# Kernel optimization log

Hardware: AMD Instinct MI355X
Metric: run time of the kernel (lower is better)

Reference implementation:

```python
import jax, jax.numpy as jnp
import numpy as np

B, NA, NT, P, DA, DM, H = 1, 4096, 1024, 32768, 128, 512, 4
DH = DA // H
DF = 4 * DA
WINDOW = 16


def _layer_norm(x, g=None, b=None, eps=1e-5):
    m = jnp.mean(x, axis=-1, keepdims=True)
    v = jnp.var(x, axis=-1, keepdims=True)
    xn = (x - m) / jnp.sqrt(v + eps)
    if g is not None:
        xn = xn * g + b
    return xn


def setup_inputs() -> dict:
    key = jax.random.key(0)
    ks = jax.random.split(key, 32)
    r = lambda k, s: (jax.random.normal(k, s, dtype=jnp.float32) * 0.05)
    return {
        'q': r(ks[0], (B, NA, DA)),
        'c_atom': r(ks[1], (B, NA, DA)),
        'h_cond': r(ks[2], (B, NT, DM)),
        'p_lm': r(ks[3], (B, P, 16)),
        't_emb': r(ks[4], (B, DA)),
        'cond_proj_w': r(ks[5], (DM, DA)), 'cond_proj_b': r(ks[6], (DA,)),
        'adaln1_w': r(ks[7], (DA, 2 * DA)), 'adaln1_b': r(ks[8], (2 * DA,)),
        'adaln2_w': r(ks[9], (DA, 2 * DA)), 'adaln2_b': r(ks[10], (2 * DA,)),
        'ln_g': jnp.ones((DA,), jnp.float32), 'ln_b': jnp.zeros((DA,), jnp.float32),
        'wq': r(ks[11], (DA, DA)), 'wk': r(ks[12], (DA, DA)),
        'wv': r(ks[13], (DA, DA)), 'wg': r(ks[14], (DA, DA)),
        'wo': r(ks[15], (DA, DA)),
        'pair_w': r(ks[16], (16, H)), 'pair_b': r(ks[17], (H,)),
        'gate1_w': r(ks[18], (DA, DA)), 'gate1_b': r(ks[19], (DA,)),
        'gate2_w': r(ks[20], (DA, DA)), 'gate2_b': r(ks[21], (DA,)),
        'sw1': r(ks[22], (DA, DF)), 'sw3': r(ks[23], (DA, DF)),
        'sw2': r(ks[24], (DF, DA)),
        'p_lm_idx': jax.random.randint(ks[25], (B, P, 2), 0, NA, dtype=jnp.int32),
        'token_idx': jnp.sort(jax.random.randint(ks[26], (B, NA), 0, NT, dtype=jnp.int32), axis=-1),
    }


def _forward(q, c_atom, h_cond, p_lm, t_emb,
             cond_proj_w, cond_proj_b, adaln1_w, adaln1_b, adaln2_w, adaln2_b,
             ln_g, ln_b, wq, wk, wv, wg, wo, pair_w, pair_b,
             gate1_w, gate1_b, gate2_w, gate2_b, sw1, sw3, sw2,
             p_lm_idx, token_idx):
    Bq, N, D = q.shape
    # gather token conditioning to atoms: (B, NA, DM)
    h_atoms = jax.vmap(lambda h, t: h[t])(h_cond, token_idx)
    cond = t_emb[:, None, :] + h_atoms @ cond_proj_w + cond_proj_b  # (B, NA, DA)
    g1, b1 = jnp.split(cond @ adaln1_w + adaln1_b, 2, axis=-1)
    q_n = (1.0 + g1) * _layer_norm(q, ln_g, ln_b) + b1

    Q = (q_n @ wq).reshape(Bq, N, H, DH)
    K = (q_n @ wk).reshape(Bq, N, H, DH)
    V = (q_n @ wv).reshape(Bq, N, H, DH)
    G_flat = q_n @ wg  # (B, N, DA); permute/reshape in torch is identity on layout

    scores = jnp.einsum('bihd,bjhd->bhij', Q, K) / jnp.sqrt(jnp.float32(DH))

    # scattered pair bias: (B, P, H) -> dense (B, H, N, N)
    bias = p_lm @ pair_w + pair_b  # (B, P, H)

    def scat(idx, bb):
        return jnp.zeros((N, N, H), bb.dtype).at[idx[:, 0], idx[:, 1]].set(bb)

    pair_bias = jax.vmap(scat)(p_lm_idx, bias).transpose(0, 3, 1, 2)
    scores = scores + pair_bias

    pos = jnp.arange(N)
    window = jnp.abs(pos[:, None] - pos[None, :]) <= WINDOW  # (N, N)
    scores = jnp.where(window[None, None, :, :], scores, -jnp.inf)

    attn = jax.nn.softmax(scores, axis=-1)
    att_out = jnp.einsum('bhij,bjhd->bihd', attn, V).reshape(Bq, N, D)

    q1 = q + jax.nn.sigmoid(G_flat) * (att_out @ wo)
    q1 = q1 + jax.nn.sigmoid(c_atom @ gate1_w + gate1_b) * q1

    g2, b2 = jnp.split(cond @ adaln2_w + adaln2_b, 2, axis=-1)
    q_n2 = (1.0 + g2) * _layer_norm(q1) + b2
    swi = (jax.nn.silu(q_n2 @ sw1) * (q_n2 @ sw3)) @ sw2
    q2 = q1 + jax.nn.sigmoid(c_atom @ gate2_w + gate2_b) * swi
    return q2  # atom_pad_mask is all-ones -> final mask multiply is identity


def reference(q, c_atom, h_cond, p_lm, t_emb,
              cond_proj_w, cond_proj_b, adaln1_w, adaln1_b, adaln2_w, adaln2_b,
              ln_g, ln_b, wq, wk, wv, wg, wo, pair_w, pair_b,
              gate1_w, gate1_b, gate2_w, gate2_b, sw1, sw3, sw2,
              p_lm_idx, token_idx):
    return _forward(q, c_atom, h_cond, p_lm, t_emb,
                    cond_proj_w, cond_proj_b, adaln1_w, adaln1_b, adaln2_w, adaln2_b,
                    ln_g, ln_b, wq, wk, wv, wg, wo, pair_w, pair_b,
                    gate1_w, gate1_b, gate2_w, gate2_b, sw1, sw3, sw2,
                    p_lm_idx, token_idx)
```

## Files before the change

### kernel.cpp

```cpp
#include <hip/hip_runtime.h>
#include <math.h>

#define NA   4096
#define DA   128
#define DM   512
#define NT   1024
#define HH   4
#define DF   512
#define PP   32768
#define WIN  16
#define BAND 33

typedef __attribute__((ext_vector_type(8))) short bf16x8;
typedef __attribute__((ext_vector_type(4))) float f32x4;

__device__ __forceinline__ float sigmoidf_(float x) { return 1.0f / (1.0f + __expf(-x)); }
__device__ __forceinline__ ushort f2bf(float f) {
    union { float f; unsigned int i; } x; x.f = f;
    unsigned int r = x.i + 0x7fffu + ((x.i >> 16) & 1u);
    return (ushort)(r >> 16);
}

template<int K, int NF>
__device__ __forceinline__ void gemm_core(
    const ushort* __restrict__ Arow, const ushort* __restrict__ WTcol,
    f32x4* acc, int ko)
{
    #pragma unroll
    for (int ks = 0; ks < K / 32; ++ks) {
        bf16x8 a = *(const bf16x8*)(Arow + ks * 32 + ko);
        #pragma unroll
        for (int nf = 0; nf < NF; ++nf) {
            bf16x8 b = *(const bf16x8*)(WTcol + (size_t)nf * 16 * K + ks * 32 + ko);
            acc[nf] = __builtin_amdgcn_mfma_f32_16x16x32_bf16(a, b, acc[nf], 0, 0, 0);
        }
    }
}

__global__ __launch_bounds__(256) void k_prep(
    const float* __restrict__ hc, const float* __restrict__ ca,
    const float* __restrict__ cw, const float* __restrict__ a1, const float* __restrict__ a2,
    const float* __restrict__ wq, const float* __restrict__ wk, const float* __restrict__ wv,
    const float* __restrict__ wg, const float* __restrict__ wo,
    const float* __restrict__ g1, const float* __restrict__ g2,
    const float* __restrict__ s1, const float* __restrict__ s3, const float* __restrict__ s2,
    ushort* hcb, ushort* cab, ushort* cwT, ushort* a1T, ushort* a2T,
    ushort* wqT, ushort* wkT, ushort* wvT, ushort* wgT, ushort* woT,
    ushort* g1T, ushort* g2T, ushort* s1T, ushort* s3T, ushort* s2T,
    float* band, float* outz)
{
    __shared__ float tile[32][33];
    const int y = blockIdx.y, bx = blockIdx.x, tid = threadIdx.x;
    if (y <= 1) {
        const float4* src = (const float4*)(y == 0 ? hc : ca);
        ushort* dst = y == 0 ? hcb : cab;
        for (int i = bx * 256 + tid; i < 131072; i += 16384) {
            float4 v = src[i];
            ushort4 st; st.x = f2bf(v.x); st.y = f2bf(v.y); st.z = f2bf(v.z); st.w = f2bf(v.w);
            *(ushort4*)&dst[(size_t)i * 4] = st;
        }
        return;
    }
    if (y == 15) {
        float4 z = {0.f, 0.f, 0.f, 0.f};
        float4* b4 = (float4*)band;
        for (int i = bx * 256 + tid; i < 135168; i += 16384) b4[i] = z;
        return;
    }
    if (y == 16) {
        float4 z = {0.f, 0.f, 0.f, 0.f};
        float4* o4 = (float4*)outz;
        for (int i = bx * 256 + tid; i < 131072; i += 16384) o4[i] = z;
        return;
    }
    const float* src; ushort* dst; int K, N;
    switch (y) {
        case 2:  src = cw; dst = cwT; K = 512; N = 128; break;
        case 3:  src = a1; dst = a1T; K = 128; N = 256; break;
        case 4:  src = a2; dst = a2T; K = 128; N = 256; break;
        case 5:  src = wq; dst = wqT; K = 128; N = 128; break;
        case 6:  src = wk; dst = wkT; K = 128; N = 128; break;
        case 7:  src = wv; dst = wvT; K = 128; N = 128; break;
        case 8:  src = wg; dst = wgT; K = 128; N = 128; break;
        case 9:  src = wo; dst = woT; K = 128; N = 128; break;
        case 10: src = g1; dst = g1T; K = 128; N = 128; break;
        case 11: src = g2; dst = g2T; K = 128; N = 128; break;
        case 12: src = s1; dst = s1T; K = 128; N = 512; break;
        case 13: src = s3; dst = s3T; K = 128; N = 512; break;
        default: src = s2; dst = s2T; K = 512; N = 128; break;
    }
    const int tn_cnt = N >> 5;
    if (bx >= (K >> 5) * tn_cnt) return;
    const int k0 = (bx / tn_cnt) << 5, n0 = (bx % tn_cnt) << 5;
    {
        int r = tid >> 3, c = (tid & 7) << 2;
        float4 v = *(const float4*)&src[(size_t)(k0 + r) * N + n0 + c];
        tile[r][c + 0] = v.x; tile[r][c + 1] = v.y;
        tile[r][c + 2] = v.z; tile[r][c + 3] = v.w;
    }
    __syncthreads();
    {
        int rn = tid >> 3, ck = (tid & 7) << 2;
        ushort4 st;
        st.x = f2bf(tile[ck + 0][rn]);
        st.y = f2bf(tile[ck + 1][rn]);
        st.z = f2bf(tile[ck + 2][rn]);
        st.w = f2bf(tile[ck + 3][rn]);
        *(ushort4*)&dst[(size_t)(n0 + rn) * K + k0 + ck] = st;
    }
}

__global__ __launch_bounds__(256) void k_cond(
    const ushort* __restrict__ hcb, const int* __restrict__ tok,
    const ushort* __restrict__ cwT, const float* __restrict__ t_emb,
    const float* __restrict__ cond_b, ushort* __restrict__ cond_bf,
    const float* __restrict__ p_lm, const float* __restrict__ pair_w,
    const float* __restrict__ pair_b, const int* __restrict__ p_idx,
    float* __restrict__ band)
{
    const int tid = threadIdx.x, y = blockIdx.y;
    if (y >= 4) {
        int p = ((y - 4) * 64 + blockIdx.x) * 256 + tid;
        int i = p_idx[2 * p], j = p_idx[2 * p + 1];
        int d = j - i + WIN;
        if (d < 0 || d > 2 * WIN) return;
        float v0 = pair_b[0], v1 = pair_b[1], v2 = pair_b[2], v3 = pair_b[3];
        #pragma unroll
        for (int k = 0; k < 16; ++k) {
            float a = p_lm[p * 16 + k];
            v0 = fmaf(a, pair_w[k * 4 + 0], v0);
            v1 = fmaf(a, pair_w[k * 4 + 1], v1);
            v2 = fmaf(a, pair_w[k * 4 + 2], v2);
            v3 = fmaf(a, pair_w[k * 4 + 3], v3);
        }
        size_t base = ((size_t)i * HH) * BAND + d;
        band[base + 0 * BAND] = v0;
        band[base + 1 * BAND] = v1;
        band[base + 2 * BAND] = v2;
        band[base + 3 * BAND] = v3;
        return;
    }
    const int l = tid & 63, w = tid >> 6, cl = l & 15, ko = (l >> 4) * 8;
    const int m0 = blockIdx.x * 64, n0 = y * 32;
    const int trow = tok[m0 + w * 16 + cl];
    f32x4 acc[2] = {};
    gemm_core<512, 2>(hcb + (size_t)trow * DM, cwT + (size_t)(n0 + cl) * DM, acc, ko);
    const int r0 = m0 + w * 16 + (l >> 4) * 4;
    #pragma unroll
    for (int nf = 0; nf < 2; ++nf) {
        int col = n0 + nf * 16 + cl;
        float add = t_emb[col] + cond_b[col];
        #pragma unroll
        for (int r = 0; r < 4; ++r)
            cond_bf[(size_t)(r0 + r) * DA + col] = f2bf(acc[nf][r] + add);
    }
}

__global__ __launch_bounds__(256) void k_modgate(
    const ushort* __restrict__ cond_bf, const ushort* __restrict__ cab,
    const ushort* __restrict__ a1T, const ushort* __restrict__ a2T,
    const ushort* __restrict__ g1T, const ushort* __restrict__ g2T,
    const float* __restrict__ ad1b, const float* __restrict__ ad2b,
    const float* __restrict__ g1b, const float* __restrict__ g2b,
    float* __restrict__ gb1, float* __restrict__ gb2,
    float* __restrict__ gate1, float* __restrict__ gate2)
{
    const int tid = threadIdx.x, y = blockIdx.y;
    const int l = tid & 63, w = tid >> 6, cl = l & 15, ko = (l >> 4) * 8;
    const int m0 = blockIdx.x * 64;
    const ushort* A; const ushort* WT; const float* bias; float* O; int ldo, n0, sig;
    if (y < 4)       { A = cond_bf; WT = a1T; bias = ad1b; O = gb1;   ldo = 256; n0 = y * 64;        sig = 0; }
    else if (y < 8)  { A = cond_bf; WT = a2T; bias = ad2b; O = gb2;   ldo = 256; n0 = (y - 4) * 64;  sig = 0; }
    else if (y < 10) { A = cab;     WT = g1T; bias = g1b;  O = gate1; ldo = 128; n0 = (y - 8) * 64;  sig = 1; }
    else             { A = cab;     WT = g2T; bias = g2b;  O = gate2; ldo = 128; n0 = (y - 10) * 64; sig = 1; }
    f32x4 acc[4] = {};
    gemm_core<128, 4>(A + (size_t)(m0 + w * 16 + cl) * DA, WT + (size_t)(n0 + cl) * DA, acc, ko);
    const int r0 = m0 + w * 16 + (l >> 4) * 4;
    #pragma unroll
    for (int nf = 0; nf < 4; ++nf) {
        int col = n0 + nf * 16 + cl;
        float bb = bias[col];
        #pragma unroll
        for (int r = 0; r < 4; ++r) {
            float v = acc[nf][r] + bb;
            if (sig) v = sigmoidf_(v);
            O[(size_t)(r0 + r) * ldo + col] = v;
        }
    }
}

__global__ __launch_bounds__(256) void k_qkvg(
    const float* __restrict__ q, const float* __restrict__ gb1,
    const float* __restrict__ ln_g, const float* __restrict__ ln_b,
    const ushort* __restrict__ wqT, const ushort* __restrict__ wkT,
    const ushort* __restrict__ wvT, const ushort* __restrict__ wgT,
    float* __restrict__ Qb, float* __restrict__ Kb,
    float* __restrict__ Vb, float* __restrict__ sG)
{
    const int tid = threadIdx.x, l = tid & 63, w = tid >> 6;
    const int cl = l & 15, kq = l >> 4, ko = kq * 8;
    const int m0 = blockIdx.x * 64, n0 = blockIdx.y * 64, z = blockIdx.z;
    const int row = m0 + w * 16 + cl;

    float qv[4][8];
    float sum = 0.f, sq = 0.f;
    #pragma unroll
    for (int ks = 0; ks < 4; ++ks) {
        float4 v0 = *(const float4*)&q[(size_t)row * DA + ks * 32 + ko];
        float4 v1 = *(const float4*)&q[(size_t)row * DA + ks * 32 + ko + 4];
        qv[ks][0] = v0.x; qv[ks][1] = v0.y; qv[ks][2] = v0.z; qv[ks][3] = v0.w;
        qv[ks][4] = v1.x; qv[ks][5] = v1.y; qv[ks][6] = v1.z; qv[ks][7] = v1.w;
        sum += v0.x + v0.y + v0.z + v0.w + v1.x + v1.y + v1.z + v1.w;
        sq += v0.x * v0.x + v0.y * v0.y + v0.z * v0.z + v0.w * v0.w
            + v1.x * v1.x + v1.y * v1.y + v1.z * v1.z + v1.w * v1.w;
    }
    sum += __shfl_xor(sum, 16); sq += __shfl_xor(sq, 16);
    sum += __shfl_xor(sum, 32); sq += __shfl_xor(sq, 32);
    float mean = sum * (1.0f / DA);
    float rs = rsqrtf(sq * (1.0f / DA) - mean * mean + 1e-5f);

    bf16x8 afr[4];
    #pragma unroll
    for (int ks = 0; ks < 4; ++ks) {
        int k = ks * 32 + ko;
        float4 lg0 = *(const float4*)&ln_g[k], lg1 = *(const float4*)&ln_g[k + 4];
        float4 lb0 = *(const float4*)&ln_b[k], lb1 = *(const float4*)&ln_b[k + 4];
        float4 g0 = *(const float4*)&gb1[(size_t)row * 256 + k];
        float4 g1v = *(const float4*)&gb1[(size_t)row * 256 + k + 4];
        float4 b0 = *(const float4*)&gb1[(size_t)row * 256 + 128 + k];
        float4 b1v = *(const float4*)&gb1[(size_t)row * 256 + 128 + k + 4];
        float lg[8] = {lg0.x, lg0.y, lg0.z, lg0.w, lg1.x, lg1.y, lg1.z, lg1.w};
        float lb[8] = {lb0.x, lb0.y, lb0.z, lb0.w, lb1.x, lb1.y, lb1.z, lb1.w};
        float gg[8] = {g0.x, g0.y, g0.z, g0.w, g1v.x, g1v.y, g1v.z, g1v.w};
        float bb[8] = {b0.x, b0.y, b0.z, b0.w, b1v.x, b1v.y, b1v.z, b1v.w};
        #pragma unroll
        for (int j = 0; j < 8; ++j) {
            float xn = (qv[ks][j] - mean) * rs;
            float yv = (1.f + gg[j]) * (xn * lg[j] + lb[j]) + bb[j];
            afr[ks][j] = (short)f2bf(yv);
        }
    }

    const ushort* WT = (z == 0) ? wqT : (z == 1) ? wkT : (z == 2) ? wvT : wgT;
    float* O = (z == 0) ? Qb : (z == 1) ? Kb : (z == 2) ? Vb : sG;
    const ushort* Wc = WT + (size_t)(n0 + cl) * DA;
    f32x4 acc[4] = {};
    #pragma unroll
    for (int ks = 0; ks < 4; ++ks) {
        #pragma unroll
        for (int nf = 0; nf < 4; ++nf) {
            bf16x8 b = *(const bf16x8*)(Wc + (size_t)nf * 16 * DA + ks * 32 + ko);
            acc[nf] = __builtin_amdgcn_mfma_f32_16x16x32_bf16(afr[ks], b, acc[nf], 0, 0, 0);
        }
    }
    const int r0 = m0 + w * 16 + kq * 4;
    #pragma unroll
    for (int nf = 0; nf < 4; ++nf) {
        int col = n0 + nf * 16 + cl;
        #pragma unroll
        for (int r = 0; r < 4; ++r) {
            float v = acc[nf][r];
            if (z == 3) v = sigmoidf_(v);
            O[(size_t)(r0 + r) * DA + col] = v;
        }
    }
}

__global__ __launch_bounds__(512) void k_attnwo(
    const float* __restrict__ Qb, const float* __restrict__ Kb,
    const float* __restrict__ Vb, const float* __restrict__ band,
    const float* __restrict__ q, const float* __restrict__ sG,
    const float* __restrict__ gate1, const ushort* __restrict__ woT,
    float* __restrict__ q1)
{
    __shared__ ushort att_s[16 * 128];
    const int tid = threadIdx.x;
    const int r0 = blockIdx.x * 16;
    {
        const int g = tid >> 3, l3 = tid & 7;
        const int rl = g >> 2, h = g & 3;
        const int i = r0 + rl;
        const float scale = 0.17677669529663687f;
        float4 qr = *(const float4*)(Qb + (size_t)i * DA + h * 32 + l3 * 4);
        const float* brow = band + ((size_t)i * HH + h) * BAND;
        float s[BAND];
        float m = -1e30f;
        #pragma unroll
        for (int jo = 0; jo < BAND; ++jo) {
            int j = i - WIN + jo;
            float sv = -1e30f;
            if ((unsigned)j < NA) {
                float4 kk = *(const float4*)(Kb + (size_t)j * DA + h * 32 + l3 * 4);
                float d = 0.f;
                d = fmaf(qr.x, kk.x, d); d = fmaf(qr.y, kk.y, d);
                d = fmaf(qr.z, kk.z, d); d = fmaf(qr.w, kk.w, d);
                d += __shfl_xor(d, 1);
                d += __shfl_xor(d, 2);
                d += __shfl_xor(d, 4);
                sv = fmaf(d, scale, brow[jo]);
            }
            s[jo] = sv;
            m = fmaxf(m, sv);
        }
        float lsum = 0.f;
        #pragma unroll
        for (int jo = 0; jo < BAND; ++jo) {
            float p = __expf(s[jo] - m);
            s[jo] = p;
            lsum += p;
        }
        float inv = 1.0f / lsum;
        float4 o = {0.f, 0.f, 0.f, 0.f};
        #pragma unroll
        for (int jo = 0; jo < BAND; ++jo) {
            int j = i - WIN + jo;
            if ((unsigned)j < NA) {
                float4 v = *(const float4*)(Vb + (size_t)j * DA + h * 32 + l3 * 4);
                o.x = fmaf(s[jo], v.x, o.x);
                o.y = fmaf(s[jo], v.y, o.y);
                o.z = fmaf(s[jo], v.z, o.z);
                o.w = fmaf(s[jo], v.w, o.w);
            }
        }
        ushort4 st;
        st.x = f2bf(o.x * inv); st.y = f2bf(o.y * inv);
        st.z = f2bf(o.z * inv); st.w = f2bf(o.w * inv);
        int byte = rl * 256 + h * 64 + l3 * 8;
        byte ^= (rl & 7) << 4;
        *(ushort4*)((char*)att_s + byte) = st;
    }
    __syncthreads();
    {
        const int l = tid & 63, w = tid >> 6;
        const int cl = l & 15, kq = l >> 4, ko = kq * 8;
        const int n0 = w * 16;
        f32x4 acc = {0.f, 0.f, 0.f, 0.f};
        #pragma unroll
        for (int ks = 0; ks < 4; ++ks) {
            int byteA = cl * 256 + (ks * 32 + ko) * 2;
            byteA ^= (cl & 7) << 4;
            bf16x8 a = *(const bf16x8*)((char*)att_s + byteA);
            bf16x8 b = *(const bf16x8*)(woT + (size_t)(n0 + cl) * DA + ks * 32 + ko);
            acc = __builtin_amdgcn_mfma_f32_16x16x32_bf16(a, b, acc, 0, 0, 0);
        }
        #pragma unroll
        for (int r = 0; r < 4; ++r) {
            int row = r0 + kq * 4 + r, col = n0 + cl;
            size_t rc = (size_t)row * DA + col;
            q1[rc] = (q[rc] + sG[rc] * acc[r]) * (1.f + gate1[rc]);
        }
    }
}

__global__ __launch_bounds__(256) void k_ffn(
    const float* __restrict__ q1, const float* __restrict__ gb2,
    const float* __restrict__ gate2,
    const ushort* __restrict__ s1T, const ushort* __restrict__ s3T,
    const ushort* __restrict__ s2T, float* __restrict__ out)
{
    __shared__ ushort hbs[16 * 128];
    const int tid = threadIdx.x, l = tid & 63, w = tid >> 6;
    const int cl = l & 15, kq = l >> 4, ko = kq * 8;
    const int m0 = blockIdx.x * 16;
    const int by = blockIdx.y;
    const int row = m0 + cl;

    float qv[4][8];
    float sum = 0.f, sq = 0.f;
    #pragma unroll
    for (int ks = 0; ks < 4; ++ks) {
        float4 v0 = *(const float4*)&q1[(size_t)row * DA + ks * 32 + ko];
        float4 v1 = *(const float4*)&q1[(size_t)row * DA + ks * 32 + ko + 4];
        qv[ks][0] = v0.x; qv[ks][1] = v0.y; qv[ks][2] = v0.z; qv[ks][3] = v0.w;
        qv[ks][4] = v1.x; qv[ks][5] = v1.y; qv[ks][6] = v1.z; qv[ks][7] = v1.w;
        sum += v0.x + v0.y + v0.z + v0.w + v1.x + v1.y + v1.z + v1.w;
        sq += v0.x * v0.x + v0.y * v0.y + v0.z * v0.z + v0.w * v0.w
            + v1.x * v1.x + v1.y * v1.y + v1.z * v1.z + v1.w * v1.w;
    }
    sum += __shfl_xor(sum, 16); sq += __shfl_xor(sq, 16);
    sum += __shfl_xor(sum, 32); sq += __shfl_xor(sq, 32);
    float mean = sum * (1.0f / DA);
    float rs = rsqrtf(sq * (1.0f / DA) - mean * mean + 1e-5f);

    bf16x8 afr[4];
    #pragma unroll
    for (int ks = 0; ks < 4; ++ks) {
        int k = ks * 32 + ko;
        float4 g0 = *(const float4*)&gb2[(size_t)row * 256 + k];
        float4 g1v = *(const float4*)&gb2[(size_t)row * 256 + k + 4];
        float4 b0 = *(const float4*)&gb2[(size_t)row * 256 + 128 + k];
        float4 b1v = *(const float4*)&gb2[(size_t)row * 256 + 128 + k + 4];
        float gg[8] = {g0.x, g0.y, g0.z, g0.w, g1v.x, g1v.y, g1v.z, g1v.w};
        float bb[8] = {b0.x, b0.y, b0.z, b0.w, b1v.x, b1v.y, b1v.z, b1v.w};
        #pragma unroll
        for (int j = 0; j < 8; ++j) {
            float xn = (qv[ks][j] - mean) * rs;
            afr[ks][j] = (short)f2bf((1.f + gg[j]) * xn + bb[j]);
        }
    }

    {
        const ushort* W1 = s1T + (size_t)(by * 128 + w * 32 + cl) * DA;
        const ushort* W3 = s3T + (size_t)(by * 128 + w * 32 + cl) * DA;
        f32x4 acc1[2] = {}, acc3[2] = {};
        #pragma unroll
        for (int ks = 0; ks < 4; ++ks) {
            #pragma unroll
            for (int nf = 0; nf < 2; ++nf) {
                bf16x8 b1 = *(const bf16x8*)(W1 + (size_t)nf * 16 * DA + ks * 32 + ko);
                acc1[nf] = __builtin_amdgcn_mfma_f32_16x16x32_bf16(afr[ks], b1, acc1[nf], 0, 0, 0);
                bf16x8 b3 = *(const bf16x8*)(W3 + (size_t)nf * 16 * DA + ks * 32 + ko);
                acc3[nf] = __builtin_amdgcn_mfma_f32_16x16x32_bf16(afr[ks], b3, acc3[nf], 0, 0, 0);
            }
        }
        #pragma unroll
        for (int nf = 0; nf < 2; ++nf) {
            #pragma unroll
            for (int r = 0; r < 4; ++r) {
                float x1 = acc1[nf][r], x3 = acc3[nf][r];
                float h = x1 * sigmoidf_(x1) * x3;
                int rr = kq * 4 + r;
                int col = w * 32 + nf * 16 + cl;
                int byte = rr * 256 + col * 2;
                byte ^= (rr & 7) << 4;
                *(ushort*)((char*)hbs + byte) = f2bf(h);
            }
        }
    }
    __syncthreads();
    {
        const ushort* W2 = s2T + (size_t)(w * 32 + cl) * DF + by * 128;
        f32x4 acc[2] = {};
        #pragma unroll
        for (int ks = 0; ks < 4; ++ks) {
            int byteA = cl * 256 + (ks * 32 + ko) * 2;
            byteA ^= (cl & 7) << 4;
            bf16x8 a = *(const bf16x8*)((char*)hbs + byteA);
            #pragma unroll
            for (int nf = 0; nf < 2; ++nf) {
                bf16x8 b = *(const bf16x8*)(W2 + (size_t)nf * 16 * DF + ks * 32 + ko);
                acc[nf] = __builtin_amdgcn_mfma_f32_16x16x32_bf16(a, b, acc[nf], 0, 0, 0);
            }
        }
        #pragma unroll
        for (int nf = 0; nf < 2; ++nf) {
            #pragma unroll
            for (int r = 0; r < 4; ++r) {
                int rowg = m0 + kq * 4 + r, col = w * 32 + nf * 16 + cl;
                size_t rc = (size_t)rowg * DA + col;
                float val = gate2[rc] * acc[nf][r];
                if (by == 0) val += q1[rc];
                atomicAdd(&out[rc], val);
            }
        }
    }
}

extern "C" void kernel_launch(void* const* d_in, const int* in_sizes, int n_in,
                              void* d_out, int out_size, void* d_ws, size_t ws_size,
                              hipStream_t stream)
{
    const float* q      = (const float*)d_in[0];
    const float* c_atom = (const float*)d_in[1];
    const float* h_cond = (const float*)d_in[2];
    const float* p_lm   = (const float*)d_in[3];
    const float* t_emb  = (const float*)d_in[4];
    const float* cond_w = (const float*)d_in[5];
    const float* cond_b = (const float*)d_in[6];
    const float* ad1w   = (const float*)d_in[7];
    const float* ad1b   = (const float*)d_in[8];
    const float* ad2w   = (const float*)d_in[9];
    const float* ad2b   = (const float*)d_in[10];
    const float* ln_g   = (const float*)d_in[11];
    const float* ln_b   = (const float*)d_in[12];
    const float* wq     = (const float*)d_in[13];
    const float* wk     = (const float*)d_in[14];
    const float* wv     = (const float*)d_in[15];
    const float* wg     = (const float*)d_in[16];
    const float* wo     = (const float*)d_in[17];
    const float* pair_w = (const float*)d_in[18];
    const float* pair_b = (const float*)d_in[19];
    const float* g1w    = (const float*)d_in[20];
    const float* g1b    = (const float*)d_in[21];
    const float* g2w    = (const float*)d_in[22];
    const float* g2b    = (const float*)d_in[23];
    const float* sw1    = (const float*)d_in[24];
    const float* sw3    = (const float*)d_in[25];
    const float* sw2    = (const float*)d_in[26];
    const int*   p_idx  = (const int*)d_in[27];
    const int*   tok    = (const int*)d_in[28];
    float* out = (float*)d_out;

    size_t off = 0;
    char* base = (char*)d_ws;
    auto alloc = [&](size_t bytes) -> void* {
        void* p = base + off;
        off += (bytes + 255) & ~(size_t)255;
        return p;
    };
    ushort* hcb     = (ushort*)alloc((size_t)NT * DM * 2);
    ushort* cab     = (ushort*)alloc((size_t)NA * DA * 2);
    ushort* cwT     = (ushort*)alloc((size_t)DM * DA * 2);
    ushort* a1T     = (ushort*)alloc((size_t)256 * 128 * 2);
    ushort* a2T     = (ushort*)alloc((size_t)256 * 128 * 2);
    ushort* wqT     = (ushort*)alloc((size_t)128 * 128 * 2);
    ushort* wkT     = (ushort*)alloc((size_t)128 * 128 * 2);
    ushort* wvT     = (ushort*)alloc((size_t)128 * 128 * 2);
    ushort* wgT     = (ushort*)alloc((size_t)128 * 128 * 2);
    ushort* woT     = (ushort*)alloc((size_t)128 * 128 * 2);
    ushort* g1T     = (ushort*)alloc((size_t)128 * 128 * 2);
    ushort* g2T     = (ushort*)alloc((size_t)128 * 128 * 2);
    ushort* s1T     = (ushort*)alloc((size_t)512 * 128 * 2);
    ushort* s3T     = (ushort*)alloc((size_t)512 * 128 * 2);
    ushort* s2T     = (ushort*)alloc((size_t)128 * 512 * 2);
    ushort* cond_bf = (ushort*)alloc((size_t)NA * DA * 2);
    float*  gb1     = (float*)alloc((size_t)NA * 256 * 4);
    float*  gb2     = (float*)alloc((size_t)NA * 256 * 4);
    float*  gate1   = (float*)alloc((size_t)NA * DA * 4);
    float*  gate2   = (float*)alloc((size_t)NA * DA * 4);
    float*  Qb      = (float*)alloc((size_t)NA * DA * 4);
    float*  Kb      = (float*)alloc((size_t)NA * DA * 4);
    float*  Vb      = (float*)alloc((size_t)NA * DA * 4);
    float*  sG      = (float*)alloc((size_t)NA * DA * 4);
    float*  band    = (float*)alloc((size_t)NA * HH * BAND * 4);
    float*  q1      = (float*)alloc((size_t)NA * DA * 4);

    k_prep<<<dim3(64, 17), 256, 0, stream>>>(
        h_cond, c_atom, cond_w, ad1w, ad2w, wq, wk, wv, wg, wo,
        g1w, g2w, sw1, sw3, sw2,
        hcb, cab, cwT, a1T, a2T, wqT, wkT, wvT, wgT, woT,
        g1T, g2T, s1T, s3T, s2T, band, out);
    k_cond<<<dim3(64, 6), 256, 0, stream>>>(hcb, tok, cwT, t_emb, cond_b, cond_bf,
                                            p_lm, pair_w, pair_b, p_idx, band);
    k_modgate<<<dim3(64, 12), 256, 0, stream>>>(cond_bf, cab, a1T, a2T, g1T, g2T,
                                                ad1b, ad2b, g1b, g2b,
                                                gb1, gb2, gate1, gate2);
    k_qkvg<<<dim3(64, 2, 4), 256, 0, stream>>>(q, gb1, ln_g, ln_b,
                                               wqT, wkT, wvT, wgT, Qb, Kb, Vb, sG);
    k_attnwo<<<NA / 16, 512, 0, stream>>>(Qb, Kb, Vb, band, q, sG, gate1, woT, q1);
    k_ffn<<<dim3(NA / 16, 4), 256, 0, stream>>>(q1, gb2, gate2, s1T, s3T, s2T, out);
    (void)in_sizes; (void)n_in; (void)out_size; (void)ws_size;
}
```

Before: 198.8 us.

## Store intermediates in bf16, split LN kernel, fuse modgate pairs, drop FFN atomics

Converts the modulation, gate and sigmoid-gate buffers from fp32 to bf16, which halves their memory traffic. The layer norm moves out of k_qkvg into a separate k_ln1 kernel that writes a bf16 normalized tensor, so the four projection blocks stop recomputing it. k_modgate now computes paired GEMMs that share one A row. k_ffn becomes a single 512-thread block per 16 rows that does all of DF, removing the output zeroing pass and the atomicAdd reduction, in exchange for less grid parallelism, an extra launch and bf16 rounding error.

```diff
diff --git a/kernel.cpp b/kernel.cpp
--- a/kernel.cpp
+++ b/kernel.cpp
@@ -20,21 +20,9 @@
     unsigned int r = x.i + 0x7fffu + ((x.i >> 16) & 1u);
     return (ushort)(r >> 16);
 }
-
-template<int K, int NF>
-__device__ __forceinline__ void gemm_core(
-    const ushort* __restrict__ Arow, const ushort* __restrict__ WTcol,
-    f32x4* acc, int ko)
-{
-    #pragma unroll
-    for (int ks = 0; ks < K / 32; ++ks) {
-        bf16x8 a = *(const bf16x8*)(Arow + ks * 32 + ko);
-        #pragma unroll
-        for (int nf = 0; nf < NF; ++nf) {
-            bf16x8 b = *(const bf16x8*)(WTcol + (size_t)nf * 16 * K + ks * 32 + ko);
-            acc[nf] = __builtin_amdgcn_mfma_f32_16x16x32_bf16(a, b, acc[nf], 0, 0, 0);
-        }
-    }
+__device__ __forceinline__ float bf2f(ushort u) {
+    union { unsigned int i; float f; } x; x.i = ((unsigned int)u) << 16;
+    return x.f;
 }
 
 __global__ __launch_bounds__(256) void k_prep(
@@ -47,7 +35,7 @@
     ushort* hcb, ushort* cab, ushort* cwT, ushort* a1T, ushort* a2T,
     ushort* wqT, ushort* wkT, ushort* wvT, ushort* wgT, ushort* woT,
     ushort* g1T, ushort* g2T, ushort* s1T, ushort* s3T, ushort* s2T,
-    float* band, float* outz)
+    float* band)
 {
     __shared__ float tile[32][33];
     const int y = blockIdx.y, bx = blockIdx.x, tid = threadIdx.x;
@@ -65,12 +53,6 @@
         float4 z = {0.f, 0.f, 0.f, 0.f};
         float4* b4 = (float4*)band;
         for (int i = bx * 256 + tid; i < 135168; i += 16384) b4[i] = z;
-        return;
-    }
-    if (y == 16) {
-        float4 z = {0.f, 0.f, 0.f, 0.f};
-        float4* o4 = (float4*)outz;
-        for (int i = bx * 256 + tid; i < 131072; i += 16384) o4[i] = z;
         return;
     }
     const float* src; ushort* dst; int K, N;
@@ -110,6 +92,22 @@
     }
 }
 
+template<int K, int NF>
+__device__ __forceinline__ void gemm_core(
+    const ushort* __restrict__ Arow, const ushort* __restrict__ WTcol,
+    f32x4* acc, int ko)
+{
+    #pragma unroll
+    for (int ks = 0; ks < K / 32; ++ks) {
+        bf16x8 a = *(const bf16x8*)(Arow + ks * 32 + ko);
+        #pragma unroll
+        for (int nf = 0; nf < NF; ++nf) {
+            bf16x8 b = *(const bf16x8*)(WTcol + (size_t)nf * 16 * K + ks * 32 + ko);
+            acc[nf] = __builtin_amdgcn_mfma_f32_16x16x32_bf16(a, b, acc[nf], 0, 0, 0);
+        }
+    }
+}
+
 __global__ __launch_bounds__(256) void k_cond(
     const ushort* __restrict__ hcb, const int* __restrict__ tok,
     const ushort* __restrict__ cwT, const float* __restrict__ t_emb,
@@ -162,106 +160,106 @@
     const ushort* __restrict__ g1T, const ushort* __restrict__ g2T,
     const float* __restrict__ ad1b, const float* __restrict__ ad2b,
     const float* __restrict__ g1b, const float* __restrict__ g2b,
-    float* __restrict__ gb1, float* __restrict__ gb2,
-    float* __restrict__ gate1, float* __restrict__ gate2)
+    ushort* __restrict__ gb1, ushort* __restrict__ gb2,
+    ushort* __restrict__ gate1, ushort* __restrict__ gate2)
 {
     const int tid = threadIdx.x, y = blockIdx.y;
     const int l = tid & 63, w = tid >> 6, cl = l & 15, ko = (l >> 4) * 8;
     const int m0 = blockIdx.x * 64;
-    const ushort* A; const ushort* WT; const float* bias; float* O; int ldo, n0, sig;
-    if (y < 4)       { A = cond_bf; WT = a1T; bias = ad1b; O = gb1;   ldo = 256; n0 = y * 64;        sig = 0; }
-    else if (y < 8)  { A = cond_bf; WT = a2T; bias = ad2b; O = gb2;   ldo = 256; n0 = (y - 4) * 64;  sig = 0; }
-    else if (y < 10) { A = cab;     WT = g1T; bias = g1b;  O = gate1; ldo = 128; n0 = (y - 8) * 64;  sig = 1; }
-    else             { A = cab;     WT = g2T; bias = g2b;  O = gate2; ldo = 128; n0 = (y - 10) * 64; sig = 1; }
-    f32x4 acc[4] = {};
-    gemm_core<128, 4>(A + (size_t)(m0 + w * 16 + cl) * DA, WT + (size_t)(n0 + cl) * DA, acc, ko);
+    const int gatep = (y >= 4);
+    const int n0 = gatep ? (y - 4) * 64 : y * 64;
+    const ushort* A  = gatep ? cab : cond_bf;
+    const ushort* W1 = gatep ? g1T : a1T;
+    const ushort* W2 = gatep ? g2T : a2T;
+    const float* b1 = gatep ? g1b : ad1b;
+    const float* b2 = gatep ? g2b : ad2b;
+    ushort* O1 = gatep ? gate1 : gb1;
+    ushort* O2 = gatep ? gate2 : gb2;
+    const int ldo = gatep ? DA : 256;
+
+    const ushort* Arow = A + (size_t)(m0 + w * 16 + cl) * DA;
+    const ushort* W1c = W1 + (size_t)(n0 + cl) * DA;
+    const ushort* W2c = W2 + (size_t)(n0 + cl) * DA;
+    f32x4 acc1[4] = {}, acc2[4] = {};
+    #pragma unroll
+    for (int ks = 0; ks < 4; ++ks) {
+        bf16x8 a = *(const bf16x8*)(Arow + ks * 32 + ko);
+        #pragma unroll
+        for (int nf = 0; nf < 4; ++nf) {
+            bf16x8 w1v = *(const bf16x8*)(W1c + (size_t)nf * 16 * DA + ks * 32 + ko);
+            acc1[nf] = __builtin_amdgcn_mfma_f32_16x16x32_bf16(a, w1v, acc1[nf], 0, 0, 0);
+            bf16x8 w2v = *(const bf16x8*)(W2c + (size_t)nf * 16 * DA + ks * 32 + ko);
+            acc2[nf] = __builtin_amdgcn_mfma_f32_16x16x32_bf16(a, w2v, acc2[nf], 0, 0, 0);
+        }
+    }
     const int r0 = m0 + w * 16 + (l >> 4) * 4;
     #pragma unroll
     for (int nf = 0; nf < 4; ++nf) {
         int col = n0 + nf * 16 + cl;
-        float bb = bias[col];
+        float bb1 = b1[col], bb2 = b2[col];
         #pragma unroll
         for (int r = 0; r < 4; ++r) {
-            float v = acc[nf][r] + bb;
-            if (sig) v = sigmoidf_(v);
-            O[(size_t)(r0 + r) * ldo + col] = v;
-        }
-    }
+            float v1 = acc1[nf][r] + bb1;
+            float v2 = acc2[nf][r] + bb2;
+            if (gatep) { v1 = sigmoidf_(v1); v2 = sigmoidf_(v2); }
+            O1[(size_t)(r0 + r) * ldo + col] = f2bf(v1);
+            O2[(size_t)(r0 + r) * ldo + col] = f2bf(v2);
+        }
+    }
+}
+
+__global__ __launch_bounds__(256) void k_ln1(
+    const float* __restrict__ q, const ushort* __restrict__ gb1,
+    const float* __restrict__ ln_g, const float* __restrict__ ln_b,
+    ushort* __restrict__ qn_bf)
+{
+    const int w = threadIdx.x >> 6, l = threadIdx.x & 63;
+    const int row = blockIdx.x * 4 + w;
+    float2 xv = *(const float2*)&q[(size_t)row * DA + 2 * l];
+    float sum = xv.x + xv.y, sq = xv.x * xv.x + xv.y * xv.y;
+    #pragma unroll
+    for (int off = 1; off <= 32; off <<= 1) {
+        sum += __shfl_xor(sum, off);
+        sq  += __shfl_xor(sq,  off);
+    }
+    float m = sum * (1.0f / DA);
+    float rs = rsqrtf(sq * (1.0f / DA) - m * m + 1e-5f);
+    ushort2 gu = *(const ushort2*)&gb1[(size_t)row * 256 + 2 * l];
+    ushort2 bu = *(const ushort2*)&gb1[(size_t)row * 256 + 128 + 2 * l];
+    float2 lg = *(const float2*)&ln_g[2 * l];
+    float2 lb = *(const float2*)&ln_b[2 * l];
+    float xn0 = (xv.x - m) * rs * lg.x + lb.x;
+    float xn1 = (xv.y - m) * rs * lg.y + lb.y;
+    ushort2 st;
+    st.x = f2bf((1.f + bf2f(gu.x)) * xn0 + bf2f(bu.x));
+    st.y = f2bf((1.f + bf2f(gu.y)) * xn1 + bf2f(bu.y));
+    *(ushort2*)&qn_bf[(size_t)row * DA + 2 * l] = st;
 }
 
 __global__ __launch_bounds__(256) void k_qkvg(
-    const float* __restrict__ q, const float* __restrict__ gb1,
-    const float* __restrict__ ln_g, const float* __restrict__ ln_b,
+    const ushort* __restrict__ qn_bf,
     const ushort* __restrict__ wqT, const ushort* __restrict__ wkT,
     const ushort* __restrict__ wvT, const ushort* __restrict__ wgT,
     float* __restrict__ Qb, float* __restrict__ Kb,
-    float* __restrict__ Vb, float* __restrict__ sG)
+    float* __restrict__ Vb, ushort* __restrict__ sG)
 {
     const int tid = threadIdx.x, l = tid & 63, w = tid >> 6;
     const int cl = l & 15, kq = l >> 4, ko = kq * 8;
     const int m0 = blockIdx.x * 64, n0 = blockIdx.y * 64, z = blockIdx.z;
-    const int row = m0 + w * 16 + cl;
-
-    float qv[4][8];
-    float sum = 0.f, sq = 0.f;
-    #pragma unroll
-    for (int ks = 0; ks < 4; ++ks) {
-        float4 v0 = *(const float4*)&q[(size_t)row * DA + ks * 32 + ko];
-        float4 v1 = *(const float4*)&q[(size_t)row * DA + ks * 32 + ko + 4];
-        qv[ks][0] = v0.x; qv[ks][1] = v0.y; qv[ks][2] = v0.z; qv[ks][3] = v0.w;
-        qv[ks][4] = v1.x; qv[ks][5] = v1.y; qv[ks][6] = v1.z; qv[ks][7] = v1.w;
-        sum += v0.x + v0.y + v0.z + v0.w + v1.x + v1.y + v1.z + v1.w;
-        sq += v0.x * v0.x + v0.y * v0.y + v0.z * v0.z + v0.w * v0.w
-            + v1.x * v1.x + v1.y * v1.y + v1.z * v1.z + v1.w * v1.w;
-    }
-    sum += __shfl_xor(sum, 16); sq += __shfl_xor(sq, 16);
-    sum += __shfl_xor(sum, 32); sq += __shfl_xor(sq, 32);
-    float mean = sum * (1.0f / DA);
-    float rs = rsqrtf(sq * (1.0f / DA) - mean * mean + 1e-5f);
-
-    bf16x8 afr[4];
-    #pragma unroll
-    for (int ks = 0; ks < 4; ++ks) {
-        int k = ks * 32 + ko;
-        float4 lg0 = *(const float4*)&ln_g[k], lg1 = *(const float4*)&ln_g[k + 4];
-        float4 lb0 = *(const float4*)&ln_b[k], lb1 = *(const float4*)&ln_b[k + 4];
-        float4 g0 = *(const float4*)&gb1[(size_t)row * 256 + k];
-        float4 g1v = *(const float4*)&gb1[(size_t)row * 256 + k + 4];
-        float4 b0 = *(const float4*)&gb1[(size_t)row * 256 + 128 + k];
-        float4 b1v = *(const float4*)&gb1[(size_t)row * 256 + 128 + k + 4];
-        float lg[8] = {lg0.x, lg0.y, lg0.z, lg0.w, lg1.x, lg1.y, lg1.z, lg1.w};
-        float lb[8] = {lb0.x, lb0.y, lb0.z, lb0.w, lb1.x, lb1.y, lb1.z, lb1.w};
-        float gg[8] = {g0.x, g0.y, g0.z, g0.w, g1v.x, g1v.y, g1v.z, g1v.w};
-        float bb[8] = {b0.x, b0.y, b0.z, b0.w, b1v.x, b1v.y, b1v.z, b1v.w};
-        #pragma unroll
-        for (int j = 0; j < 8; ++j) {
-            float xn = (qv[ks][j] - mean) * rs;
-            float yv = (1.f + gg[j]) * (xn * lg[j] + lb[j]) + bb[j];
-            afr[ks][j] = (short)f2bf(yv);
-        }
-    }
-
     const ushort* WT = (z == 0) ? wqT : (z == 1) ? wkT : (z == 2) ? wvT : wgT;
-    float* O = (z == 0) ? Qb : (z == 1) ? Kb : (z == 2) ? Vb : sG;
-    const ushort* Wc = WT + (size_t)(n0 + cl) * DA;
     f32x4 acc[4] = {};
-    #pragma unroll
-    for (int ks = 0; ks < 4; ++ks) {
-        #pragma unroll
-        for (int nf = 0; nf < 4; ++nf) {
-            bf16x8 b = *(const bf16x8*)(Wc + (size_t)nf * 16 * DA + ks * 32 + ko);
-            acc[nf] = __builtin_amdgcn_mfma_f32_16x16x32_bf16(afr[ks], b, acc[nf], 0, 0, 0);
-        }
-    }
+    gemm_core<128, 4>(qn_bf + (size_t)(m0 + w * 16 + cl) * DA,
+                      WT + (size_t)(n0 + cl) * DA, acc, ko);
     const int r0 = m0 + w * 16 + kq * 4;
+    float* O = (z == 0) ? Qb : (z == 1) ? Kb : Vb;
     #pragma unroll
     for (int nf = 0; nf < 4; ++nf) {
         int col = n0 + nf * 16 + cl;
         #pragma unroll
         for (int r = 0; r < 4; ++r) {
-            float v = acc[nf][r];
-            if (z == 3) v = sigmoidf_(v);
-            O[(size_t)(r0 + r) * DA + col] = v;
+            size_t rc = (size_t)(r0 + r) * DA + col;
+            if (z == 3) sG[rc] = f2bf(sigmoidf_(acc[nf][r]));
+            else O[rc] = acc[nf][r];
         }
     }
 }
@@ -269,8 +267,8 @@
 __global__ __launch_bounds__(512) void k_attnwo(
     const float* __restrict__ Qb, const float* __restrict__ Kb,
     const float* __restrict__ Vb, const float* __restrict__ band,
-    const float* __restrict__ q, const float* __restrict__ sG,
-    const float* __restrict__ gate1, const ushort* __restrict__ woT,
+    const float* __restrict__ q, const ushort* __restrict__ sG,
+    const ushort* __restrict__ gate1, const ushort* __restrict__ woT,
     float* __restrict__ q1)
 {
     __shared__ ushort att_s[16 * 128];
@@ -347,22 +345,21 @@
         for (int r = 0; r < 4; ++r) {
             int row = r0 + kq * 4 + r, col = n0 + cl;
             size_t rc = (size_t)row * DA + col;
-            q1[rc] = (q[rc] + sG[rc] * acc[r]) * (1.f + gate1[rc]);
-        }
-    }
-}
-
-__global__ __launch_bounds__(256) void k_ffn(
-    const float* __restrict__ q1, const float* __restrict__ gb2,
-    const float* __restrict__ gate2,
+            q1[rc] = (q[rc] + bf2f(sG[rc]) * acc[r]) * (1.f + bf2f(gate1[rc]));
+        }
+    }
+}
+
+__global__ __launch_bounds__(512) void k_ffn(
+    const float* __restrict__ q1, const ushort* __restrict__ gb2,
+    const ushort* __restrict__ gate2,
     const ushort* __restrict__ s1T, const ushort* __restrict__ s3T,
     const ushort* __restrict__ s2T, float* __restrict__ out)
 {
-    __shared__ ushort hbs[16 * 128];
+    __shared__ ushort hbs[16 * 512];
     const int tid = threadIdx.x, l = tid & 63, w = tid >> 6;
     const int cl = l & 15, kq = l >> 4, ko = kq * 8;
     const int m0 = blockIdx.x * 16;
-    const int by = blockIdx.y;
     const int row = m0 + cl;
 
     float qv[4][8];
@@ -386,12 +383,14 @@
     #pragma unroll
     for (int ks = 0; ks < 4; ++ks) {
         int k = ks * 32 + ko;
-        float4 g0 = *(const float4*)&gb2[(size_t)row * 256 + k];
-        float4 g1v = *(const float4*)&gb2[(size_t)row * 256 + k + 4];
-        float4 b0 = *(const float4*)&gb2[(size_t)row * 256 + 128 + k];
-        float4 b1v = *(const float4*)&gb2[(size_t)row * 256 + 128 + k + 4];
-        float gg[8] = {g0.x, g0.y, g0.z, g0.w, g1v.x, g1v.y, g1v.z, g1v.w};
-        float bb[8] = {b0.x, b0.y, b0.z, b0.w, b1v.x, b1v.y, b1v.z, b1v.w};
+        ushort4 g0 = *(const ushort4*)&gb2[(size_t)row * 256 + k];
+        ushort4 g1v = *(const ushort4*)&gb2[(size_t)row * 256 + k + 4];
+        ushort4 b0 = *(const ushort4*)&gb2[(size_t)row * 256 + 128 + k];
+        ushort4 b1v = *(const ushort4*)&gb2[(size_t)row * 256 + 128 + k + 4];
+        float gg[8] = {bf2f(g0.x), bf2f(g0.y), bf2f(g0.z), bf2f(g0.w),
+                       bf2f(g1v.x), bf2f(g1v.y), bf2f(g1v.z), bf2f(g1v.w)};
+        float bb[8] = {bf2f(b0.x), bf2f(b0.y), bf2f(b0.z), bf2f(b0.w),
+                       bf2f(b1v.x), bf2f(b1v.y), bf2f(b1v.z), bf2f(b1v.w)};
         #pragma unroll
         for (int j = 0; j < 8; ++j) {
             float xn = (qv[ks][j] - mean) * rs;
@@ -400,13 +399,14 @@
     }
 
     {
-        const ushort* W1 = s1T + (size_t)(by * 128 + w * 32 + cl) * DA;
-        const ushort* W3 = s3T + (size_t)(by * 128 + w * 32 + cl) * DA;
-        f32x4 acc1[2] = {}, acc3[2] = {};
+        const int c0 = w * 64;
+        const ushort* W1 = s1T + (size_t)(c0 + cl) * DA;
+        const ushort* W3 = s3T + (size_t)(c0 + cl) * DA;
+        f32x4 acc1[4] = {}, acc3[4] = {};
         #pragma unroll
         for (int ks = 0; ks < 4; ++ks) {
             #pragma unroll
-            for (int nf = 0; nf < 2; ++nf) {
+            for (int nf = 0; nf < 4; ++nf) {
                 bf16x8 b1 = *(const bf16x8*)(W1 + (size_t)nf * 16 * DA + ks * 32 + ko);
                 acc1[nf] = __builtin_amdgcn_mfma_f32_16x16x32_bf16(afr[ks], b1, acc1[nf], 0, 0, 0);
                 bf16x8 b3 = *(const bf16x8*)(W3 + (size_t)nf * 16 * DA + ks * 32 + ko);
@@ -414,14 +414,14 @@
             }
         }
         #pragma unroll
-        for (int nf = 0; nf < 2; ++nf) {
+        for (int nf = 0; nf < 4; ++nf) {
             #pragma unroll
             for (int r = 0; r < 4; ++r) {
                 float x1 = acc1[nf][r], x3 = acc3[nf][r];
                 float h = x1 * sigmoidf_(x1) * x3;
                 int rr = kq * 4 + r;
-                int col = w * 32 + nf * 16 + cl;
-                int byte = rr * 256 + col * 2;
+                int col = c0 + nf * 16 + cl;
+                int byte = rr * 1024 + col * 2;
                 byte ^= (rr & 7) << 4;
                 *(ushort*)((char*)hbs + byte) = f2bf(h);
             }
@@ -429,29 +429,22 @@
     }
     __syncthreads();
     {
-        const ushort* W2 = s2T + (size_t)(w * 32 + cl) * DF + by * 128;
-        f32x4 acc[2] = {};
-        #pragma unroll
-        for (int ks = 0; ks < 4; ++ks) {
-            int byteA = cl * 256 + (ks * 32 + ko) * 2;
+        const int n0 = w * 16;
+        const ushort* W2 = s2T + (size_t)(n0 + cl) * DF;
+        f32x4 acc = {0.f, 0.f, 0.f, 0.f};
+        #pragma unroll
+        for (int ks = 0; ks < 16; ++ks) {
+            int byteA = cl * 1024 + (ks * 32 + ko) * 2;
             byteA ^= (cl & 7) << 4;
             bf16x8 a = *(const bf16x8*)((char*)hbs + byteA);
-            #pragma unroll
-            for (int nf = 0; nf < 2; ++nf) {
-                bf16x8 b = *(const bf16x8*)(W2 + (size_t)nf * 16 * DF + ks * 32 + ko);
-                acc[nf] = __builtin_amdgcn_mfma_f32_16x16x32_bf16(a, b, acc[nf], 0, 0, 0);
-            }
-        }
-        #pragma unroll
-        for (int nf = 0; nf < 2; ++nf) {
-            #pragma unroll
-            for (int r = 0; r < 4; ++r) {
-                int rowg = m0 + kq * 4 + r, col = w * 32 + nf * 16 + cl;
-                size_t rc = (size_t)rowg * DA + col;
-                float val = gate2[rc] * acc[nf][r];
-                if (by == 0) val += q1[rc];
-                atomicAdd(&out[rc], val);
-            }
+            bf16x8 b = *(const bf16x8*)(W2 + ks * 32 + ko);
+            acc = __builtin_amdgcn_mfma_f32_16x16x32_bf16(a, b, acc, 0, 0, 0);
+        }
+        #pragma unroll
+        for (int r = 0; r < 4; ++r) {
+            int rowg = m0 + kq * 4 + r, col = n0 + cl;
+            size_t rc = (size_t)rowg * DA + col;
+            out[rc] = q1[rc] + bf2f(gate2[rc]) * acc[r];
         }
     }
 }
@@ -514,30 +507,31 @@
     ushort* s3T     = (ushort*)alloc((size_t)512 * 128 * 2);
     ushort* s2T     = (ushort*)alloc((size_t)128 * 512 * 2);
     ushort* cond_bf = (ushort*)alloc((size_t)NA * DA * 2);
-    float*  gb1     = (float*)alloc((size_t)NA * 256 * 4);
-    float*  gb2     = (float*)alloc((size_t)NA * 256 * 4);
-    float*  gate1   = (float*)alloc((size_t)NA * DA * 4);
-    float*  gate2   = (float*)alloc((size_t)NA * DA * 4);
+    ushort* gb1     = (ushort*)alloc((size_t)NA * 256 * 2);
+    ushort* gb2     = (ushort*)alloc((size_t)NA * 256 * 2);
+    ushort* gate1   = (ushort*)alloc((size_t)NA * DA * 2);
+    ushort* gate2   = (ushort*)alloc((size_t)NA * DA * 2);
+    ushort* qn_bf   = (ushort*)alloc((size_t)NA * DA * 2);
     float*  Qb      = (float*)alloc((size_t)NA * DA * 4);
     float*  Kb      = (float*)alloc((size_t)NA * DA * 4);
     float*  Vb      = (float*)alloc((size_t)NA * DA * 4);
-    float*  sG      = (float*)alloc((size_t)NA * DA * 4);
+    ushort* sG      = (ushort*)alloc((size_t)NA * DA * 2);
     float*  band    = (float*)alloc((size_t)NA * HH * BAND * 4);
     float*  q1      = (float*)alloc((size_t)NA * DA * 4);
 
-    k_prep<<<dim3(64, 17), 256, 0, stream>>>(
+    k_prep<<<dim3(64, 16), 256, 0, stream>>>(
         h_cond, c_atom, cond_w, ad1w, ad2w, wq, wk, wv, wg, wo,
         g1w, g2w, sw1, sw3, sw2,
         hcb, cab, cwT, a1T, a2T, wqT, wkT, wvT, wgT, woT,
-        g1T, g2T, s1T, s3T, s2T, band, out);
+        g1T, g2T, s1T, s3T, s2T, band);
     k_cond<<<dim3(64, 6), 256, 0, stream>>>(hcb, tok, cwT, t_emb, cond_b, cond_bf,
                                             p_lm, pair_w, pair_b, p_idx, band);
-    k_modgate<<<dim3(64, 12), 256, 0, stream>>>(cond_bf, cab, a1T, a2T, g1T, g2T,
-                                                ad1b, ad2b, g1b, g2b,
-                                                gb1, gb2, gate1, gate2);
-    k_qkvg<<<dim3(64, 2, 4), 256, 0, stream>>>(q, gb1, ln_g, ln_b,
-                                               wqT, wkT, wvT, wgT, Qb, Kb, Vb, sG);
+    k_modgate<<<dim3(64, 6), 256, 0, stream>>>(cond_bf, cab, a1T, a2T, g1T, g2T,
+                                               ad1b, ad2b, g1b, g2b,
+                                               gb1, gb2, gate1, gate2);
+    k_ln1<<<NA / 4, 256, 0, stream>>>(q, gb1, ln_g, ln_b, qn_bf);
+    k_qkvg<<<dim3(64, 2, 4), 256, 0, stream>>>(qn_bf, wqT, wkT, wvT, wgT, Qb, Kb, Vb, sG);
     k_attnwo<<<NA / 16, 512, 0, stream>>>(Qb, Kb, Vb, band, q, sG, gate1, woT, q1);
-    k_ffn<<<dim3(NA / 16, 4), 256, 0, stream>>>(q1, gb2, gate2, s1T, s3T, s2T, out);
+    k_ffn<<<NA / 16, 512, 0, stream>>>(q1, gb2, gate2, s1T, s3T, s2T, out);
     (void)in_sizes; (void)n_in; (void)out_size; (void)ws_size;
 }
```

Result: faster. 186.7 us (-6.1%).
